# Optimization experiments

Hardware: AMD Instinct MI355X
Metric: run time of the kernel (lower is better)

## Reference

```python
import jax, jax.numpy as jnp
import numpy as np

SCALE = 4.0  # VeRA scale hyperparameter


def setup_inputs() -> dict:
    key = jax.random.key(0)
    ks = jax.random.split(key, 7)
    T, IN, OUT, R = 8192, 4096, 4096, 256
    return {
        "x": jax.random.normal(ks[0], (T, IN), dtype=jnp.float32),
        "base_weight": jax.random.normal(ks[1], (OUT, IN), dtype=jnp.float32) * 0.02,
        "base_bias": jax.random.normal(ks[2], (OUT,), dtype=jnp.float32) * 0.02,
        "vera_random_A": jax.random.normal(ks[3], (R, IN), dtype=jnp.float32) * (1.0 / np.sqrt(IN)),
        "vera_random_B": jax.random.normal(ks[4], (OUT, R), dtype=jnp.float32) * (1.0 / np.sqrt(R)),
        "vera_d": jax.random.normal(ks[5], (R,), dtype=jnp.float32) * 0.01,
        "vera_b": 0.1 * jnp.ones((OUT,), dtype=jnp.float32),
    }


def reference(x, base_weight, base_bias, vera_random_A, vera_random_B, vera_d, vera_b):
    # delta_W = scale * diag(vera_b) @ B @ diag(vera_d) @ A  -> row/col scaling, no diag matmuls
    # shapes: B (out, r), A (r, in), delta (out, in)
    delta = SCALE * jnp.einsum("or,ri->oi", vera_b[:, None] * vera_random_B, vera_d[:, None] * vera_random_A)
    # linear: y = x @ (W + delta)^T + bias
    return x @ (base_weight + delta).T + base_bias
```

## Files before the change

### kernel.cpp

```cpp
#include <hip/hip_runtime.h>


typedef __attribute__((ext_vector_type(8))) short short8;
typedef __attribute__((ext_vector_type(4))) float f32x4;

__device__ __forceinline__ unsigned short f2bf(float f) {
  union { float f; unsigned int u; } c; c.f = f;
  unsigned int u = c.u;
  unsigned int r = (u + 0x7fffu + ((u >> 16) & 1u)) >> 16;
  return (unsigned short)r;
}

__device__ __forceinline__ void gl2lds16(const unsigned short* g, unsigned short* l) {
  __builtin_amdgcn_global_load_lds(
      (const __attribute__((address_space(1))) unsigned int*)g,
      (__attribute__((address_space(3))) unsigned int*)l, 16, 0, 0);
}

__global__ __launch_bounds__(256) void k_pre(const float* __restrict__ x,
                                             unsigned short* __restrict__ xb,
                                             const float* __restrict__ Bv,
                                             const float* __restrict__ Av,
                                             const float* __restrict__ dv,
                                             const float* __restrict__ bv,
                                             unsigned short* __restrict__ Bd,
                                             unsigned short* __restrict__ AbT) {
  __shared__ float tl[32][33];
  const int blk = blockIdx.x;
  const int tid = threadIdx.x;
  if (blk < 8192) {
#pragma unroll
    for (int s = 0; s < 4; ++s) {
      int i = blk * 1024 + s * 256 + tid;
      const float4 v = ((const float4*)x)[i];
      union { unsigned short u[4]; unsigned long long ll; } o;
      o.u[0] = f2bf(v.x); o.u[1] = f2bf(v.y); o.u[2] = f2bf(v.z); o.u[3] = f2bf(v.w);
      ((unsigned long long*)xb)[i] = o.ll;
    }
  } else if (blk < 12288) {
    int idx = (blk - 8192) * 256 + tid;
    int o = idx >> 8, r = idx & 255;
    Bd[idx] = f2bf(4.0f * bv[o] * Bv[idx] * dv[r]);
  } else {
    int blk2 = blk - 12288;
    int ti = blk2 >> 3;
    int tr = blk2 & 7;
#pragma unroll
    for (int s = 0; s < 4; ++s) {
      int r = tr * 32 + s * 8 + (tid >> 5);
      int i = ti * 32 + (tid & 31);
      tl[s * 8 + (tid >> 5)][tid & 31] = Av[(size_t)r * 4096 + i];
    }
    __syncthreads();
#pragma unroll
    for (int s = 0; s < 4; ++s) {
      int iloc = s * 8 + (tid >> 5);
      int rloc = tid & 31;
      AbT[(size_t)(ti * 32 + iloc) * 256 + tr * 32 + rloc] = f2bf(tl[rloc][iloc]);
    }
  }
}

template <int FOLD>
__global__ __launch_bounds__(512, 2) void gemm256(const unsigned short* __restrict__ Amat,
                                                  const unsigned short* __restrict__ Bmat,
                                                  int K, int N, int NBY,
                                                  const float* __restrict__ extra,
                                                  float* __restrict__ outF,
                                                  unsigned short* __restrict__ outB) {
  __shared__ __align__(16) unsigned short As[2 * 2 * 8192];
  __shared__ __align__(16) unsigned short Bs[2 * 2 * 8192];

  const int tid  = threadIdx.x;
  const int lane = tid & 63;
  const int wave = tid >> 6;
  const int wm   = wave >> 2;
  const int wn   = wave & 3;
  const int quad = lane >> 4;
  const int m16  = lane & 15;
  const int qsl  = quad ^ ((m16 >> 1) & 3);

  const int nwg  = gridDim.x;
  const int cpx  = nwg >> 3;
  const int wgid = (blockIdx.x & 7) * cpx + (blockIdx.x >> 3);
  const int by   = wgid % NBY;
  const int bx   = wgid / NBY;
  const int blockM = by * 256;
  const int blockN = bx * 256;

  const int srow = tid >> 2;
  const int sq8  = ((tid & 3) ^ ((tid >> 3) & 3)) * 8;
  const size_t aB0 = (size_t)(blockM + srow) * K + sq8;
  const size_t aB1 = aB0 + (size_t)128 * K;
  const size_t bB0 = (size_t)(blockN + srow) * K + sq8;
  const size_t bB1 = bB0 + (size_t)128 * K;

  const short8* Asv = (const short8*)As;
  const short8* Bsv = (const short8*)Bs;
  const int aRd = wm * 512 + m16 * 4 + qsl;
  const int bRd = wn * 256 + m16 * 4 + qsl;

  f32x4 acc[8][4];
#pragma unroll
  for (int i = 0; i < 8; ++i)
#pragma unroll
    for (int j = 0; j < 4; ++j) acc[i][j] = (f32x4){0.f, 0.f, 0.f, 0.f};

  short8 afr[4], bfr[4];

#define WAITV(n) asm volatile("s_waitcnt vmcnt(" #n ") lgkmcnt(0)" ::: "memory")

#define ISSUE_A(bufi, kh, koff) do {                                         \
    unsigned short* d_ = As + ((bufi) * 2 + (kh)) * 8192 + tid * 8;          \
    gl2lds16(Amat + aB0 + (koff) + (kh) * 32, d_);                           \
    gl2lds16(Amat + aB1 + (koff) + (kh) * 32, d_ + 4096);                    \
  } while (0)

#define ISSUE_B(bufi, kh, koff) do {                                         \
    unsigned short* d_ = Bs + ((bufi) * 2 + (kh)) * 8192 + tid * 8;          \
    gl2lds16(Bmat + bB0 + (koff) + (kh) * 32, d_);                           \
    gl2lds16(Bmat + bB1 + (koff) + (kh) * 32, d_ + 4096);                    \
  } while (0)

#define RD_B(Bb, h) do {                                                     \
    _Pragma("unroll") for (int nt = 0; nt < 4; ++nt)                         \
      bfr[nt] = Bsv[((Bb) * 2 + (h)) * 1024 + bRd + nt * 64];                \
  } while (0)

#define RD_A(Bb, h, mh) do {                                                 \
    _Pragma("unroll") for (int mt = 0; mt < 4; ++mt)                         \
      afr[mt] = Asv[((Bb) * 2 + (h)) * 1024 + aRd + (mh) * 256 + mt * 64];   \
  } while (0)

#define MM(mh) do {                                                          \
    __builtin_amdgcn_s_setprio(1);                                           \
    _Pragma("unroll") for (int mt = 0; mt < 4; ++mt)                         \
    _Pragma("unroll") for (int nt = 0; nt < 4; ++nt)                         \
      acc[(mh) * 4 + mt][nt] = __builtin_amdgcn_mfma_f32_16x16x32_bf16(      \
          afr[mt], bfr[nt], acc[(mh) * 4 + mt][nt], 0, 0, 0);                \
    __builtin_amdgcn_s_setprio(0);                                           \
  } while (0)

#define TILE(Bb, ko, W1, W3, I12, I34) do {                                  \
    WAITV(W1);                                                               \
    __builtin_amdgcn_s_barrier();                                            \
    if (I12) ISSUE_A((Bb) ^ 1, 1, (ko) + 64);                                \
    RD_B(Bb, 0); RD_A(Bb, 0, 0); MM(0);                                      \
    if (I12) ISSUE_B((Bb) ^ 1, 1, (ko) + 64);                                \
    RD_A(Bb, 0, 1); MM(1);                                                   \
    WAITV(W3);                                                               \
    __builtin_amdgcn_s_barrier();                                            \
    if (I34) ISSUE_A(Bb, 0, (ko) + 128);                                     \
    RD_B(Bb, 1); RD_A(Bb, 1, 0); MM(0);                                      \
    if (I34) ISSUE_B(Bb, 0, (ko) + 128);                                     \
    RD_A(Bb, 1, 1); MM(1);                                                   \
  } while (0)

  ISSUE_A(0, 0, (size_t)0);  ISSUE_B(0, 0, (size_t)0);
  ISSUE_A(0, 1, (size_t)0);  ISSUE_B(0, 1, (size_t)0);
  ISSUE_A(1, 0, (size_t)64); ISSUE_B(1, 0, (size_t)64);

  const int NT = K >> 6;
  size_t ko = 0;
  for (int t = 0; t < NT - 2; t += 2) {
    TILE(0, ko, 8, 8, 1, 1);
    TILE(1, ko + 64, 8, 8, 1, 1);
    ko += 128;
  }
  TILE(0, ko, 8, 8, 1, 0);
  TILE(1, ko + 64, 4, 0, 0, 0);

#undef WAITV
#undef ISSUE_A
#undef ISSUE_B
#undef RD_B
#undef RD_A
#undef MM
#undef TILE

#pragma unroll
  for (int mt = 0; mt < 8; ++mt) {
    const int row0 = blockM + wm * 128 + mt * 16 + quad * 4;
#pragma unroll
    for (int nt = 0; nt < 4; ++nt) {
      const int col = blockN + wn * 64 + nt * 16 + m16;
      f32x4 v = acc[mt][nt];
      if (FOLD) {
#pragma unroll
        for (int r = 0; r < 4; ++r) {
          size_t o = (size_t)(row0 + r) * N + col;
          outB[o] = f2bf(extra[o] + v[r]);
        }
      } else {
        const float bb = extra[col];
#pragma unroll
        for (int r = 0; r < 4; ++r) {
          size_t o = (size_t)(row0 + r) * N + col;
          outF[o] = v[r] + bb;
        }
      }
    }
  }
}

extern "C" void kernel_launch(void* const* d_in, const int* in_sizes, int n_in,
                              void* d_out, int out_size, void* d_ws, size_t ws_size,
                              hipStream_t stream) {
  const float* x    = (const float*)d_in[0];
  const float* W    = (const float*)d_in[1];
  const float* bias = (const float*)d_in[2];
  const float* A    = (const float*)d_in[3];
  const float* B    = (const float*)d_in[4];
  const float* dv   = (const float*)d_in[5];
  const float* bv   = (const float*)d_in[6];
  float* out = (float*)d_out;

  char* ws = (char*)d_ws;
  unsigned short* xb  = (unsigned short*)ws;
  unsigned short* Wc  = (unsigned short*)(ws + (size_t)(64 << 20));
  unsigned short* Bd  = (unsigned short*)(ws + (size_t)(96 << 20));
  unsigned short* AbT = (unsigned short*)(ws + (size_t)(98 << 20));

  hipLaunchKernelGGL(k_pre, dim3(13312), dim3(256), 0, stream,
                     x, xb, B, A, dv, bv, Bd, AbT);
  hipLaunchKernelGGL((gemm256<1>), dim3(256), dim3(512), 0, stream,
                     Bd, AbT, 256, 4096, 16, W, (float*)nullptr, Wc);
  hipLaunchKernelGGL((gemm256<0>), dim3(512), dim3(512), 0, stream,
                     xb, Wc, 4096, 4096, 32, bias, out, (unsigned short*)nullptr);
}
```

Measured before the change: 547.5 us.

## Restructure GEMM main loop into 8-phase ping-pong schedule with reordered tile mapping

Rewrites the bf16 GEMM inner loop as eight phases per two K-tiles. Each phase reads LDS fragments, issues one global-to-LDS prefetch, and then passes a barrier before a 16-MFMA burst with explicit sched_barriers. B fragments for both k-halves are held in registers (bfr[8]), and waits become vmcnt-only at quarter boundaries. Workgroup-to-tile mapping switches from column-major to row-major over N tiles, and the main GEMM is launched with NBX=16. The aim is better overlap of loads with MFMA and better cache locality, at the cost of extra barriers and register pressure.

```diff
diff --git a/kernel.cpp b/kernel.cpp
--- a/kernel.cpp
+++ b/kernel.cpp
@@ -64,7 +64,7 @@
 template <int FOLD>
 __global__ __launch_bounds__(512, 2) void gemm256(const unsigned short* __restrict__ Amat,
                                                   const unsigned short* __restrict__ Bmat,
-                                                  int K, int N, int NBY,
+                                                  int K, int N, int NBX,
                                                   const float* __restrict__ extra,
                                                   float* __restrict__ outF,
                                                   unsigned short* __restrict__ outB) {
@@ -83,8 +83,8 @@
   const int nwg  = gridDim.x;
   const int cpx  = nwg >> 3;
   const int wgid = (blockIdx.x & 7) * cpx + (blockIdx.x >> 3);
-  const int by   = wgid % NBY;
-  const int bx   = wgid / NBY;
+  const int bx   = wgid % NBX;
+  const int by   = wgid / NBX;
   const int blockM = by * 256;
   const int blockN = bx * 256;
 
@@ -106,9 +106,12 @@
 #pragma unroll
     for (int j = 0; j < 4; ++j) acc[i][j] = (f32x4){0.f, 0.f, 0.f, 0.f};
 
-  short8 afr[4], bfr[4];
-
-#define WAITV(n) asm volatile("s_waitcnt vmcnt(" #n ") lgkmcnt(0)" ::: "memory")
+  short8 afr[4];
+  short8 bfr[8];
+
+#define VM4()  asm volatile("s_waitcnt vmcnt(4)" ::: "memory")
+#define VM0()  asm volatile("s_waitcnt vmcnt(0)" ::: "memory")
+#define NOPW() ((void)0)
 
 #define ISSUE_A(bufi, kh, koff) do {                                         \
     unsigned short* d_ = As + ((bufi) * 2 + (kh)) * 8192 + tid * 8;          \
@@ -122,61 +125,80 @@
     gl2lds16(Bmat + bB1 + (koff) + (kh) * 32, d_ + 4096);                    \
   } while (0)
 
-#define RD_B(Bb, h) do {                                                     \
+#define RD_B8(Bb) do {                                                       \
+    _Pragma("unroll") for (int kh = 0; kh < 2; ++kh)                         \
     _Pragma("unroll") for (int nt = 0; nt < 4; ++nt)                         \
-      bfr[nt] = Bsv[((Bb) * 2 + (h)) * 1024 + bRd + nt * 64];                \
-  } while (0)
-
-#define RD_A(Bb, h, mh) do {                                                 \
-    _Pragma("unroll") for (int mt = 0; mt < 4; ++mt)                         \
-      afr[mt] = Asv[((Bb) * 2 + (h)) * 1024 + aRd + (mh) * 256 + mt * 64];   \
-  } while (0)
-
-#define MM(mh) do {                                                          \
+      bfr[kh * 4 + nt] = Bsv[((Bb) * 2 + kh) * 1024 + bRd + nt * 64];        \
+  } while (0)
+
+#define RD_A4(Bb, q) do {                                                    \
+    _Pragma("unroll") for (int kh = 0; kh < 2; ++kh)                         \
+    _Pragma("unroll") for (int mt = 0; mt < 2; ++mt)                         \
+      afr[kh * 2 + mt] =                                                     \
+          Asv[((Bb) * 2 + kh) * 1024 + aRd + (q) * 128 + mt * 64];           \
+  } while (0)
+
+#define MM16(q) do {                                                         \
+    _Pragma("unroll") for (int kh = 0; kh < 2; ++kh)                         \
+    _Pragma("unroll") for (int mt = 0; mt < 2; ++mt)                         \
+    _Pragma("unroll") for (int nt = 0; nt < 4; ++nt)                         \
+      acc[(q) * 2 + mt][nt] = __builtin_amdgcn_mfma_f32_16x16x32_bf16(       \
+          afr[kh * 2 + mt], bfr[kh * 4 + nt], acc[(q) * 2 + mt][nt], 0, 0, 0);\
+  } while (0)
+
+#define PH(Bb, q, STAGE, WAITOPT) do {                                       \
+    if ((q) == 0) { RD_B8(Bb); }                                             \
+    RD_A4(Bb, q);                                                            \
+    STAGE;                                                                   \
+    WAITOPT;                                                                 \
+    asm volatile("s_barrier" ::: "memory");                                  \
+    asm volatile("s_waitcnt lgkmcnt(0)" ::: "memory");                       \
+    __builtin_amdgcn_sched_barrier(0);                                       \
     __builtin_amdgcn_s_setprio(1);                                           \
-    _Pragma("unroll") for (int mt = 0; mt < 4; ++mt)                         \
-    _Pragma("unroll") for (int nt = 0; nt < 4; ++nt)                         \
-      acc[(mh) * 4 + mt][nt] = __builtin_amdgcn_mfma_f32_16x16x32_bf16(      \
-          afr[mt], bfr[nt], acc[(mh) * 4 + mt][nt], 0, 0, 0);                \
+    MM16(q);                                                                 \
     __builtin_amdgcn_s_setprio(0);                                           \
-  } while (0)
-
-#define TILE(Bb, ko, W1, W3, I12, I34) do {                                  \
-    WAITV(W1);                                                               \
-    __builtin_amdgcn_s_barrier();                                            \
-    if (I12) ISSUE_A((Bb) ^ 1, 1, (ko) + 64);                                \
-    RD_B(Bb, 0); RD_A(Bb, 0, 0); MM(0);                                      \
-    if (I12) ISSUE_B((Bb) ^ 1, 1, (ko) + 64);                                \
-    RD_A(Bb, 0, 1); MM(1);                                                   \
-    WAITV(W3);                                                               \
-    __builtin_amdgcn_s_barrier();                                            \
-    if (I34) ISSUE_A(Bb, 0, (ko) + 128);                                     \
-    RD_B(Bb, 1); RD_A(Bb, 1, 0); MM(0);                                      \
-    if (I34) ISSUE_B(Bb, 0, (ko) + 128);                                     \
-    RD_A(Bb, 1, 1); MM(1);                                                   \
-  } while (0)
-
-  ISSUE_A(0, 0, (size_t)0);  ISSUE_B(0, 0, (size_t)0);
-  ISSUE_A(0, 1, (size_t)0);  ISSUE_B(0, 1, (size_t)0);
-  ISSUE_A(1, 0, (size_t)64); ISSUE_B(1, 0, (size_t)64);
+    __builtin_amdgcn_sched_barrier(0);                                       \
+    asm volatile("s_barrier" ::: "memory");                                  \
+  } while (0)
+
+  ISSUE_A(0, 0, (size_t)0);  ISSUE_A(0, 1, (size_t)0);
+  ISSUE_B(0, 0, (size_t)0);  ISSUE_B(0, 1, (size_t)0);
+  ISSUE_B(1, 0, (size_t)64); ISSUE_B(1, 1, (size_t)64);
+  VM4();
+  asm volatile("s_barrier" ::: "memory");
 
   const int NT = K >> 6;
+  const int NI = NT >> 1;
   size_t ko = 0;
-  for (int t = 0; t < NT - 2; t += 2) {
-    TILE(0, ko, 8, 8, 1, 1);
-    TILE(1, ko + 64, 8, 8, 1, 1);
+  for (int i = 0; i < NI - 1; ++i) {
+    PH(0, 0, ISSUE_A(1, 0, ko + 64),  NOPW());
+    PH(0, 1, ISSUE_A(1, 1, ko + 64),  NOPW());
+    PH(0, 2, ISSUE_B(0, 0, ko + 128), NOPW());
+    PH(0, 3, ISSUE_B(0, 1, ko + 128), VM4());
+    PH(1, 0, ISSUE_A(0, 0, ko + 128), NOPW());
+    PH(1, 1, ISSUE_A(0, 1, ko + 128), NOPW());
+    PH(1, 2, ISSUE_B(1, 0, ko + 192), NOPW());
+    PH(1, 3, ISSUE_B(1, 1, ko + 192), VM4());
     ko += 128;
   }
-  TILE(0, ko, 8, 8, 1, 0);
-  TILE(1, ko + 64, 4, 0, 0, 0);
-
-#undef WAITV
+  PH(0, 0, ISSUE_A(1, 0, ko + 64), NOPW());
+  PH(0, 1, ISSUE_A(1, 1, ko + 64), NOPW());
+  PH(0, 2, NOPW(), NOPW());
+  PH(0, 3, NOPW(), VM0());
+  PH(1, 0, NOPW(), NOPW());
+  PH(1, 1, NOPW(), NOPW());
+  PH(1, 2, NOPW(), NOPW());
+  PH(1, 3, NOPW(), NOPW());
+
+#undef VM4
+#undef VM0
+#undef NOPW
 #undef ISSUE_A
 #undef ISSUE_B
-#undef RD_B
-#undef RD_A
-#undef MM
-#undef TILE
+#undef RD_B8
+#undef RD_A4
+#undef MM16
+#undef PH
 
 #pragma unroll
   for (int mt = 0; mt < 8; ++mt) {
@@ -226,5 +248,5 @@
   hipLaunchKernelGGL((gemm256<1>), dim3(256), dim3(512), 0, stream,
                      Bd, AbT, 256, 4096, 16, W, (float*)nullptr, Wc);
   hipLaunchKernelGGL((gemm256<0>), dim3(512), dim3(512), 0, stream,
-                     xb, Wc, 4096, 4096, 32, bias, out, (unsigned short*)nullptr);
-}
+                     xb, Wc, 4096, 4096, 16, bias, out, (unsigned short*)nullptr);
+}
```

Measured after the change: 553.5 us. About the same (+1.1%).
